# Performance work log

Measured on AMD Instinct MI355X. Metric: run time of the kernel, lower is better.

## Reference

```python
import jax, jax.numpy as jnp
import numpy as np

N_EMBD = 2048
N_HEAD = 16
N_KV_HEAD = 4
HD = N_EMBD // N_HEAD  # 128
B, T = 1, 4096
EPS = 1e-6


def apply_rope(x, cos, sin):
    # x: [B,T,H,hd]; cos/sin: [T,1,hd//2]
    hd = x.shape[-1] // 2
    x1, x2 = x[..., :hd], x[..., hd:]
    y1 = x1 * cos + x2 * sin
    y2 = x2 * cos - x1 * sin
    return jnp.concatenate((y1, y2), axis=-1).astype(x.dtype)


def rms_norm(x, eps=EPS):
    return x * jax.lax.rsqrt(jnp.mean(jnp.square(x), axis=-1, keepdims=True) + eps)


def setup_inputs() -> dict:
    key = jax.random.key(0)
    ks = jax.random.split(key, 7)
    s = 0.02
    return {
        "x": jax.random.normal(ks[0], (B, T, N_EMBD), dtype=jnp.float32),
        "cos": jax.random.normal(ks[1], (T, 1, HD // 2), dtype=jnp.float32),
        "sin": jax.random.normal(ks[2], (T, 1, HD // 2), dtype=jnp.float32),
        "wq": jax.random.normal(ks[3], (N_EMBD, N_HEAD * HD), dtype=jnp.float32) * s,
        "wk": jax.random.normal(ks[4], (N_EMBD, N_KV_HEAD * HD), dtype=jnp.float32) * s,
        "wv": jax.random.normal(ks[5], (N_EMBD, N_KV_HEAD * HD), dtype=jnp.float32) * s,
        "wo": jax.random.normal(ks[6], (N_EMBD, N_EMBD), dtype=jnp.float32) * s,
    }


def reference(x, cos, sin, wq, wk, wv, wo):
    Bb, Tt, C = x.shape
    q = (x @ wq).reshape(Bb, Tt, N_HEAD, HD)
    k = (x @ wk).reshape(Bb, Tt, N_KV_HEAD, HD)
    v = (x @ wv).reshape(Bb, Tt, N_KV_HEAD, HD)
    q = rms_norm(apply_rope(q, cos, sin))
    k = rms_norm(apply_rope(k, cos, sin))
    g = N_HEAD // N_KV_HEAD
    if g > 1:
        k = jnp.repeat(k, g, axis=2)  # [B,T,H,hd]
        v = jnp.repeat(v, g, axis=2)
    scale = 1.0 / jnp.sqrt(jnp.float32(HD))
    # scores: [B,H,T,S]
    scores = jnp.einsum("bthd,bshd->bhts", q, k) * scale
    causal = jnp.tril(jnp.ones((Tt, Tt), dtype=bool))
    scores = jnp.where(causal, scores, jnp.finfo(scores.dtype).min)
    attn = jax.nn.softmax(scores, axis=-1)
    y = jnp.einsum("bhts,bshd->bthd", attn, v).reshape(Bb, Tt, C)
    return y @ wo
```

## Files before the change

### kernel.cpp

```cpp
#include <hip/hip_runtime.h>

#define T_SEQ 4096
#define C_EMB 2048
#define NH 16
#define NKV 4
#define HD 128

typedef short bf16x8 __attribute__((ext_vector_type(8)));
typedef float f32x4 __attribute__((ext_vector_type(4)));
typedef unsigned short u16x4 __attribute__((ext_vector_type(4)));

__device__ inline unsigned short f2bf(float f) {
    unsigned int u = __float_as_uint(f);
    unsigned int r = (u + 0x7FFFu + ((u >> 16) & 1u)) >> 16;
    return (unsigned short)r;
}

__device__ __forceinline__ void async_cp16(const unsigned short* g, unsigned short* l) {
    __builtin_amdgcn_global_load_lds((const __attribute__((address_space(1))) unsigned int*)g,
                                     (__attribute__((address_space(3))) unsigned int*)l,
                                     16, 0, 0);
}

__global__ __launch_bounds__(256) void cvt_bf16(const float* __restrict__ in,
                                                unsigned short* __restrict__ out, int n) {
    int i = (blockIdx.x * 256 + threadIdx.x) * 4;
    if (i >= n) return;
    float4 f = *(const float4*)(&in[i]);
    u16x4 o;
    o.x = f2bf(f.x); o.y = f2bf(f.y); o.z = f2bf(f.z); o.w = f2bf(f.w);
    *(u16x4*)(&out[i]) = o;
}

__global__ __launch_bounds__(256) void transpose_all(const float* __restrict__ wq,
                                                     const float* __restrict__ wk,
                                                     const float* __restrict__ wv,
                                                     const float* __restrict__ wo,
                                                     unsigned short* __restrict__ wqkvT,
                                                     unsigned short* __restrict__ woT) {
    __shared__ float tile[32][33];
    int z = blockIdx.z;
    const float* in;
    unsigned short* out;
    int ld_in;
    if (z == 0)      { in = wq; out = wqkvT;                         ld_in = 2048; }
    else if (z == 1) { in = wk; out = wqkvT + (size_t)2048 * 2048;   ld_in = 512;  }
    else if (z == 2) { in = wv; out = wqkvT + (size_t)2560 * 2048;   ld_in = 512;  }
    else             { in = wo; out = woT;                           ld_in = 2048; }
    if ((z == 1 || z == 2) && blockIdx.x >= 16) return;

    int x = blockIdx.x * 32 + threadIdx.x;
    for (int i = threadIdx.y; i < 32; i += 8) {
        int y = blockIdx.y * 32 + i;
        tile[i][threadIdx.x] = in[(size_t)y * ld_in + x];
    }
    __syncthreads();
    int xo = blockIdx.y * 32 + threadIdx.x;
    for (int i = threadIdx.y; i < 32; i += 8) {
        int yo = blockIdx.x * 32 + i;
        out[(size_t)yo * 2048 + xo] = f2bf(tile[threadIdx.x][i]);
    }
}

__global__ __launch_bounds__(256, 4) void gemm_qkv(const unsigned short* __restrict__ A,
                                                   const unsigned short* __restrict__ Bt,
                                                   const float* __restrict__ cosb,
                                                   const float* __restrict__ sinb,
                                                   unsigned short* __restrict__ Qn,
                                                   unsigned short* __restrict__ Kn,
                                                   unsigned short* __restrict__ Vt) {
    __shared__ __align__(16) unsigned short As[2][128 * 32];
    __shared__ __align__(16) unsigned short Bs[2][128 * 32];
    const int K = 2048;
    int t = threadIdx.x;
    int w = t >> 6, lane = t & 63;
    int ln = lane & 15, q = lane >> 4;
    int wm = w * 32;
    int m0 = blockIdx.y * 128, n0 = blockIdx.x * 128;

    f32x4 acc[2][8] = {};

#pragma unroll
    for (int s = 0; s < 2; ++s) {
        int L = s * 256 + t;
        int r = L >> 2;
        int c = (L & 3) ^ ((L >> 4) & 3);
        async_cp16(&A[(size_t)(m0 + r) * K + c * 8], &As[0][s * 2048 + w * 512]);
        async_cp16(&Bt[(size_t)(n0 + r) * K + c * 8], &Bs[0][s * 2048 + w * 512]);
    }

    for (int it = 0; it < 64; ++it) {
        __syncthreads();
        if (it < 63) {
            int k0 = (it + 1) * 32;
            int p = (it + 1) & 1;
#pragma unroll
            for (int s = 0; s < 2; ++s) {
                int L = s * 256 + t;
                int r = L >> 2;
                int c = (L & 3) ^ ((L >> 4) & 3);
                async_cp16(&A[(size_t)(m0 + r) * K + k0 + c * 8], &As[p][s * 2048 + w * 512]);
                async_cp16(&Bt[(size_t)(n0 + r) * K + k0 + c * 8], &Bs[p][s * 2048 + w * 512]);
            }
        }
        int p = it & 1;
        int cs = (q ^ ((ln >> 2) & 3)) * 8;
        bf16x8 af[2], bfr[8];
#pragma unroll
        for (int i = 0; i < 2; ++i) af[i] = *(const bf16x8*)(&As[p][(wm + i * 16 + ln) * 32 + cs]);
#pragma unroll
        for (int j = 0; j < 8; ++j) bfr[j] = *(const bf16x8*)(&Bs[p][(j * 16 + ln) * 32 + cs]);
#pragma unroll
        for (int i = 0; i < 2; ++i)
#pragma unroll
            for (int j = 0; j < 8; ++j)
                acc[i][j] = __builtin_amdgcn_mfma_f32_16x16x32_bf16(af[i], bfr[j], acc[i][j], 0, 0, 0);
    }

    if (n0 < 2560) {
        bool isQ = (n0 < 2048);
        int h = isQ ? (n0 >> 7) : ((n0 - 2048) >> 7);
#pragma unroll
        for (int i = 0; i < 2; ++i)
#pragma unroll
            for (int r = 0; r < 4; ++r) {
                int row = m0 + wm + i * 16 + q * 4 + r;
                float y1[4], y2[4];
                float ss = 0.0f;
#pragma unroll
                for (int j = 0; j < 4; ++j) {
                    float a = acc[i][j][r];
                    float b = acc[i][j + 4][r];
                    float cc = cosb[row * 64 + j * 16 + ln];
                    float sv = sinb[row * 64 + j * 16 + ln];
                    y1[j] = a * cc + b * sv;
                    y2[j] = b * cc - a * sv;
                    ss += y1[j] * y1[j] + y2[j] * y2[j];
                }
                ss += __shfl_xor(ss, 1);
                ss += __shfl_xor(ss, 2);
                ss += __shfl_xor(ss, 4);
                ss += __shfl_xor(ss, 8);
                float rv = rsqrtf(ss * (1.0f / 128.0f) + 1e-6f);
                if (isQ) {
                    float s = rv * (0.08838834764831845f * 1.4426950408889634f);
                    unsigned short* ob = Qn + (size_t)row * 2048 + h * 128;
#pragma unroll
                    for (int j = 0; j < 4; ++j) {
                        ob[j * 16 + ln] = f2bf(y1[j] * s);
                        ob[64 + j * 16 + ln] = f2bf(y2[j] * s);
                    }
                } else {
                    unsigned short* ob = Kn + (size_t)row * 512 + h * 128;
#pragma unroll
                    for (int j = 0; j < 4; ++j) {
                        ob[j * 16 + ln] = f2bf(y1[j] * rv);
                        ob[64 + j * 16 + ln] = f2bf(y2[j] * rv);
                    }
                }
            }
    } else {
        int v0 = n0 - 2560;
        unsigned short* sm = &As[0][0];
#pragma unroll
        for (int half = 0; half < 2; ++half) {
            __syncthreads();
#pragma unroll
            for (int i = 0; i < 2; ++i)
#pragma unroll
                for (int jj = 0; jj < 4; ++jj) {
                    int j = half * 4 + jj;
                    int cc = jj * 16 + ln;
                    int rr = wm + i * 16 + q * 4;
                    u16x4 pk;
                    pk.x = f2bf(acc[i][j][0]); pk.y = f2bf(acc[i][j][1]);
                    pk.z = f2bf(acc[i][j][2]); pk.w = f2bf(acc[i][j][3]);
                    *(u16x4*)(&sm[cc * 136 + rr]) = pk;
                }
            __syncthreads();
            int vtr = t >> 2, mseg = (t & 3) * 32;
            unsigned short* dst = Vt + (size_t)(v0 + half * 64 + vtr) * 4096 + m0 + mseg;
            const unsigned short* src = &sm[vtr * 136 + mseg];
            *(int4*)(dst)      = *(const int4*)(src);
            *(int4*)(dst + 8)  = *(const int4*)(src + 8);
            *(int4*)(dst + 16) = *(const int4*)(src + 16);
            *(int4*)(dst + 24) = *(const int4*)(src + 24);
        }
    }
}

__global__ __launch_bounds__(256, 4) void gemm_bt_db(const unsigned short* __restrict__ A,
                                                     const unsigned short* __restrict__ Bt,
                                                     float* __restrict__ C, int M, int N, int K) {
    __shared__ __align__(16) unsigned short As[2][128 * 32];
    __shared__ __align__(16) unsigned short Bs[2][128 * 32];
    int t = threadIdx.x;
    int w = t >> 6, lane = t & 63;
    int ln = lane & 15, q = lane >> 4;
    int wm = (w >> 1) * 64, wn = (w & 1) * 64;
    int m0 = blockIdx.y * 128, n0 = blockIdx.x * 128;

    f32x4 acc[4][4] = {};

#pragma unroll
    for (int s = 0; s < 2; ++s) {
        int L = s * 256 + t;
        int r = L >> 2;
        int c = (L & 3) ^ ((L >> 4) & 3);
        async_cp16(&A[(size_t)(m0 + r) * K + c * 8], &As[0][s * 2048 + w * 512]);
        async_cp16(&Bt[(size_t)(n0 + r) * K + c * 8], &Bs[0][s * 2048 + w * 512]);
    }

    int niter = K >> 5;
    for (int it = 0; it < niter; ++it) {
        __syncthreads();
        if (it < niter - 1) {
            int k0 = (it + 1) * 32;
            int p = (it + 1) & 1;
#pragma unroll
            for (int s = 0; s < 2; ++s) {
                int L = s * 256 + t;
                int r = L >> 2;
                int c = (L & 3) ^ ((L >> 4) & 3);
                async_cp16(&A[(size_t)(m0 + r) * K + k0 + c * 8], &As[p][s * 2048 + w * 512]);
                async_cp16(&Bt[(size_t)(n0 + r) * K + k0 + c * 8], &Bs[p][s * 2048 + w * 512]);
            }
        }
        int p = it & 1;
        int cs = (q ^ ((ln >> 2) & 3)) * 8;
        bf16x8 af[4], bfr[4];
#pragma unroll
        for (int i = 0; i < 4; ++i) af[i] = *(const bf16x8*)(&As[p][(wm + i * 16 + ln) * 32 + cs]);
#pragma unroll
        for (int j = 0; j < 4; ++j) bfr[j] = *(const bf16x8*)(&Bs[p][(wn + j * 16 + ln) * 32 + cs]);
#pragma unroll
        for (int i = 0; i < 4; ++i)
#pragma unroll
            for (int j = 0; j < 4; ++j)
                acc[i][j] = __builtin_amdgcn_mfma_f32_16x16x32_bf16(af[i], bfr[j], acc[i][j], 0, 0, 0);
    }
#pragma unroll
    for (int i = 0; i < 4; ++i)
#pragma unroll
        for (int j = 0; j < 4; ++j)
#pragma unroll
            for (int r = 0; r < 4; ++r) {
                int row = m0 + wm + i * 16 + q * 4 + r;
                int col = n0 + wn + j * 16 + ln;
                C[(size_t)row * N + col] = acc[i][j][r];
            }
}

__global__ __launch_bounds__(256) void flash_attn(const unsigned short* __restrict__ Qn,
                                                  const unsigned short* __restrict__ Kn,
                                                  const unsigned short* __restrict__ Vt,
                                                  unsigned short* __restrict__ Ao) {
    __shared__ __align__(16) unsigned short Ks[2][64 * 128];
    __shared__ __align__(16) unsigned short Vs[2][128 * 64];
    __shared__ __align__(16) unsigned short Pl[4][16 * 72];

    int pairi = blockIdx.x;
    int h = blockIdx.y;
    int kvh = h >> 2;
    int t = threadIdx.x;
    int w = t >> 6, lane = t & 63;
    int ln = lane & 15, q = lane >> 4;

    int nA = 64 - pairi;
    int bq = 63 - pairi;
    int wq0 = bq * 64 + w * 16;

    bf16x8 qf[4];
    {
        const unsigned short* qb = Qn + (size_t)(wq0 + ln) * 2048 + h * 128;
#pragma unroll
        for (int kc = 0; kc < 4; ++kc) qf[kc] = *(const bf16x8*)(qb + kc * 32 + q * 8);
    }

    f32x4 o[8] = {};
    f32x4 l_p = {0.f, 0.f, 0.f, 0.f};

#pragma unroll
    for (int s = 0; s < 4; ++s) {
        int L = s * 256 + t;
        int key = L >> 4;
        int c = (L & 15) ^ (key & 15);
        async_cp16(Kn + (size_t)key * 512 + kvh * 128 + c * 8, &Ks[0][s * 2048 + w * 512]);
    }
#pragma unroll
    for (int s = 0; s < 4; ++s) {
        int L = s * 256 + t;
        int hd = L >> 3;
        int c = (L & 7) ^ (hd & 7);
        async_cp16(Vt + (size_t)(kvh * 128 + hd) * 4096 + c * 8, &Vs[0][s * 2048 + w * 512]);
    }

    for (int it = 0; it < 65; ++it) {
        __syncthreads();

        int nxt = it + 1;
        if (nxt < 65) {
            int nkt = (nxt < nA) ? nxt * 64 : (nxt - nA) * 64;
            unsigned short* kd = Ks[nxt & 1];
            unsigned short* vd = Vs[nxt & 1];
#pragma unroll
            for (int s = 0; s < 4; ++s) {
                int L = s * 256 + t;
                int key = L >> 4;
                int c = (L & 15) ^ (key & 15);
                async_cp16(Kn + (size_t)(nkt + key) * 512 + kvh * 128 + c * 8,
                           kd + s * 2048 + w * 512);
            }
#pragma unroll
            for (int s = 0; s < 4; ++s) {
                int L = s * 256 + t;
                int hd = L >> 3;
                int c = (L & 7) ^ (hd & 7);
                async_cp16(Vt + (size_t)(kvh * 128 + hd) * 4096 + nkt + c * 8,
                           vd + s * 2048 + w * 512);
            }
        }

        if (it == nA) {
#pragma unroll
            for (int r = 0; r < 4; ++r) {
                float lsum = l_p[r];
                lsum += __shfl_xor(lsum, 1);
                lsum += __shfl_xor(lsum, 2);
                lsum += __shfl_xor(lsum, 4);
                lsum += __shfl_xor(lsum, 8);
                float inv = 1.0f / lsum;
                int row = wq0 + q * 4 + r;
                unsigned short* ob = Ao + (size_t)row * 2048 + h * 128;
#pragma unroll
                for (int f = 0; f < 8; ++f) ob[f * 16 + ln] = f2bf(o[f][r] * inv);
            }
            bq = pairi;
            wq0 = bq * 64 + w * 16;
            const unsigned short* qb = Qn + (size_t)(wq0 + ln) * 2048 + h * 128;
#pragma unroll
            for (int kc = 0; kc < 4; ++kc) qf[kc] = *(const bf16x8*)(qb + kc * 32 + q * 8);
#pragma unroll
            for (int f = 0; f < 8; ++f) o[f] = (f32x4){0.f, 0.f, 0.f, 0.f};
            l_p = (f32x4){0.f, 0.f, 0.f, 0.f};
        }

        int kt0 = (it < nA) ? it * 64 : (it - nA) * 64;
        const unsigned short* kb = Ks[it & 1];
        const unsigned short* vb = Vs[it & 1];

        f32x4 sA[4] = {{-16.6f, -16.6f, -16.6f, -16.6f}, {-16.6f, -16.6f, -16.6f, -16.6f},
                       {-16.6f, -16.6f, -16.6f, -16.6f}, {-16.6f, -16.6f, -16.6f, -16.6f}};
#pragma unroll
        for (int jt = 0; jt < 4; ++jt) {
            int key = jt * 16 + ln;
#pragma unroll
            for (int kc = 0; kc < 4; ++kc) {
                int cs = ((kc * 4 + q) ^ ln) * 8;
                bf16x8 kf = *(const bf16x8*)(&kb[key * 128 + cs]);
                sA[jt] = __builtin_amdgcn_mfma_f32_16x16x32_bf16(qf[kc], kf, sA[jt], 0, 0, 0);
            }
        }
        if (kt0 + 63 > wq0) {
#pragma unroll
            for (int jt = 0; jt < 4; ++jt)
#pragma unroll
                for (int r = 0; r < 4; ++r) {
                    int key = kt0 + jt * 16 + ln;
                    int row = wq0 + q * 4 + r;
                    if (key > row) sA[jt][r] = -3e38f;
                }
        }
#pragma unroll
        for (int r = 0; r < 4; ++r) {
            int prow = (q * 4 + r) * 72;
#pragma unroll
            for (int jt = 0; jt < 4; ++jt) {
                float p = __builtin_amdgcn_exp2f(sA[jt][r]);
                Pl[w][prow + jt * 16 + ln] = (unsigned short)(__float_as_uint(p) >> 16);
                l_p[r] += p;
            }
        }

#pragma unroll
        for (int ks = 0; ks < 2; ++ks) {
            bf16x8 pa = *(const bf16x8*)(&Pl[w][ln * 72 + ks * 32 + q * 8]);
            int cs = ((ks * 4 + q) ^ (ln & 7)) * 8;
#pragma unroll
            for (int f = 0; f < 8; ++f) {
                bf16x8 vf = *(const bf16x8*)(&vb[(f * 16 + ln) * 64 + cs]);
                o[f] = __builtin_amdgcn_mfma_f32_16x16x32_bf16(pa, vf, o[f], 0, 0, 0);
            }
        }
    }
#pragma unroll
    for (int r = 0; r < 4; ++r) {
        float lsum = l_p[r];
        lsum += __shfl_xor(lsum, 1);
        lsum += __shfl_xor(lsum, 2);
        lsum += __shfl_xor(lsum, 4);
        lsum += __shfl_xor(lsum, 8);
        float inv = 1.0f / lsum;
        int row = wq0 + q * 4 + r;
        unsigned short* ob = Ao + (size_t)row * 2048 + h * 128;
#pragma unroll
        for (int f = 0; f < 8; ++f) ob[f * 16 + ln] = f2bf(o[f][r] * inv);
    }
}

extern "C" void kernel_launch(void* const* d_in, const int* in_sizes, int n_in,
                              void* d_out, int out_size, void* d_ws, size_t ws_size,
                              hipStream_t stream) {
    const float* x    = (const float*)d_in[0];
    const float* cosb = (const float*)d_in[1];
    const float* sinb = (const float*)d_in[2];
    const float* wq   = (const float*)d_in[3];
    const float* wk   = (const float*)d_in[4];
    const float* wv   = (const float*)d_in[5];
    const float* wo   = (const float*)d_in[6];
    float* out = (float*)d_out;

    char* ws = (char*)d_ws;
    unsigned short* xb    = (unsigned short*)ws;
    unsigned short* wqkvT = xb    + (size_t)4096 * 2048;
    unsigned short* woT   = wqkvT + (size_t)3072 * 2048;
    unsigned short* Qn    = woT   + (size_t)2048 * 2048;
    unsigned short* Kn    = Qn    + (size_t)4096 * 2048;
    unsigned short* Vt    = Kn    + (size_t)4096 * 512;
    unsigned short* Ao    = Vt    + (size_t)512 * 4096;

    cvt_bf16<<<(4096 * 2048 / 4 + 255) / 256, 256, 0, stream>>>(x, xb, 4096 * 2048);
    transpose_all<<<dim3(64, 64, 4), dim3(32, 8), 0, stream>>>(wq, wk, wv, wo, wqkvT, woT);
    gemm_qkv<<<dim3(24, 32), 256, 0, stream>>>(xb, wqkvT, cosb, sinb, Qn, Kn, Vt);
    flash_attn<<<dim3(32, 16), 256, 0, stream>>>(Qn, Kn, Vt, Ao);
    gemm_bt_db<<<dim3(16, 32), 256, 0, stream>>>(Ao, woT, out, 4096, 2048, 2048);
}
```

Before: 357.5 us.

## Make each attention wave own 32 query rows with 2 waves per block

The flash attention kernel now runs 128 threads (2 waves) per block, and each wave handles 32 query rows as two 16-row sub-tiles instead of one. Every K and V fragment read from LDS is reused across two MFMAs, which halves LDS read traffic per unit of compute. The cost is twice the accumulator and Q registers per wave, only two waves per block to hide latency, and each thread issuing twice as many async copies. The grid is unchanged at 512 blocks, so each CU has fewer waves resident.

```diff
diff --git a/kernel.cpp b/kernel.cpp
--- a/kernel.cpp
+++ b/kernel.cpp
@@ -251,13 +251,13 @@
             }
 }
 
-__global__ __launch_bounds__(256) void flash_attn(const unsigned short* __restrict__ Qn,
+__global__ __launch_bounds__(128) void flash_attn(const unsigned short* __restrict__ Qn,
                                                   const unsigned short* __restrict__ Kn,
                                                   const unsigned short* __restrict__ Vt,
                                                   unsigned short* __restrict__ Ao) {
     __shared__ __align__(16) unsigned short Ks[2][64 * 128];
     __shared__ __align__(16) unsigned short Vs[2][128 * 64];
-    __shared__ __align__(16) unsigned short Pl[4][16 * 72];
+    __shared__ __align__(16) unsigned short Pl[2][32 * 72];
 
     int pairi = blockIdx.x;
     int h = blockIdx.y;
@@ -268,31 +268,32 @@
 
     int nA = 64 - pairi;
     int bq = 63 - pairi;
-    int wq0 = bq * 64 + w * 16;
-
-    bf16x8 qf[4];
-    {
-        const unsigned short* qb = Qn + (size_t)(wq0 + ln) * 2048 + h * 128;
-#pragma unroll
-        for (int kc = 0; kc < 4; ++kc) qf[kc] = *(const bf16x8*)(qb + kc * 32 + q * 8);
-    }
-
-    f32x4 o[8] = {};
-    f32x4 l_p = {0.f, 0.f, 0.f, 0.f};
-
-#pragma unroll
-    for (int s = 0; s < 4; ++s) {
-        int L = s * 256 + t;
+    int wq0 = bq * 64 + w * 32;
+
+    bf16x8 qf[2][4];
+#pragma unroll
+    for (int i = 0; i < 2; ++i) {
+        const unsigned short* qb = Qn + (size_t)(wq0 + i * 16 + ln) * 2048 + h * 128;
+#pragma unroll
+        for (int kc = 0; kc < 4; ++kc) qf[i][kc] = *(const bf16x8*)(qb + kc * 32 + q * 8);
+    }
+
+    f32x4 o[2][8] = {};
+    f32x4 l_p[2] = {};
+
+#pragma unroll
+    for (int s = 0; s < 8; ++s) {
+        int L = s * 128 + t;
         int key = L >> 4;
         int c = (L & 15) ^ (key & 15);
-        async_cp16(Kn + (size_t)key * 512 + kvh * 128 + c * 8, &Ks[0][s * 2048 + w * 512]);
-    }
-#pragma unroll
-    for (int s = 0; s < 4; ++s) {
-        int L = s * 256 + t;
+        async_cp16(Kn + (size_t)key * 512 + kvh * 128 + c * 8, &Ks[0][s * 1024 + w * 512]);
+    }
+#pragma unroll
+    for (int s = 0; s < 8; ++s) {
+        int L = s * 128 + t;
         int hd = L >> 3;
         int c = (L & 7) ^ (hd & 7);
-        async_cp16(Vt + (size_t)(kvh * 128 + hd) * 4096 + c * 8, &Vs[0][s * 2048 + w * 512]);
+        async_cp16(Vt + (size_t)(kvh * 128 + hd) * 4096 + c * 8, &Vs[0][s * 1024 + w * 512]);
     }
 
     for (int it = 0; it < 65; ++it) {
@@ -304,53 +305,66 @@
             unsigned short* kd = Ks[nxt & 1];
             unsigned short* vd = Vs[nxt & 1];
 #pragma unroll
-            for (int s = 0; s < 4; ++s) {
-                int L = s * 256 + t;
+            for (int s = 0; s < 8; ++s) {
+                int L = s * 128 + t;
                 int key = L >> 4;
                 int c = (L & 15) ^ (key & 15);
                 async_cp16(Kn + (size_t)(nkt + key) * 512 + kvh * 128 + c * 8,
-                           kd + s * 2048 + w * 512);
-            }
-#pragma unroll
-            for (int s = 0; s < 4; ++s) {
-                int L = s * 256 + t;
+                           kd + s * 1024 + w * 512);
+            }
+#pragma unroll
+            for (int s = 0; s < 8; ++s) {
+                int L = s * 128 + t;
                 int hd = L >> 3;
                 int c = (L & 7) ^ (hd & 7);
                 async_cp16(Vt + (size_t)(kvh * 128 + hd) * 4096 + nkt + c * 8,
-                           vd + s * 2048 + w * 512);
+                           vd + s * 1024 + w * 512);
             }
         }
 
         if (it == nA) {
 #pragma unroll
-            for (int r = 0; r < 4; ++r) {
-                float lsum = l_p[r];
-                lsum += __shfl_xor(lsum, 1);
-                lsum += __shfl_xor(lsum, 2);
-                lsum += __shfl_xor(lsum, 4);
-                lsum += __shfl_xor(lsum, 8);
-                float inv = 1.0f / lsum;
-                int row = wq0 + q * 4 + r;
-                unsigned short* ob = Ao + (size_t)row * 2048 + h * 128;
-#pragma unroll
-                for (int f = 0; f < 8; ++f) ob[f * 16 + ln] = f2bf(o[f][r] * inv);
-            }
+            for (int i = 0; i < 2; ++i)
+#pragma unroll
+                for (int r = 0; r < 4; ++r) {
+                    float lsum = l_p[i][r];
+                    lsum += __shfl_xor(lsum, 1);
+                    lsum += __shfl_xor(lsum, 2);
+                    lsum += __shfl_xor(lsum, 4);
+                    lsum += __shfl_xor(lsum, 8);
+                    float inv = 1.0f / lsum;
+                    int row = wq0 + i * 16 + q * 4 + r;
+                    unsigned short* ob = Ao + (size_t)row * 2048 + h * 128;
+#pragma unroll
+                    for (int f = 0; f < 8; ++f) ob[f * 16 + ln] = f2bf(o[i][f][r] * inv);
+                }
             bq = pairi;
-            wq0 = bq * 64 + w * 16;
-            const unsigned short* qb = Qn + (size_t)(wq0 + ln) * 2048 + h * 128;
-#pragma unroll
-            for (int kc = 0; kc < 4; ++kc) qf[kc] = *(const bf16x8*)(qb + kc * 32 + q * 8);
-#pragma unroll
-            for (int f = 0; f < 8; ++f) o[f] = (f32x4){0.f, 0.f, 0.f, 0.f};
-            l_p = (f32x4){0.f, 0.f, 0.f, 0.f};
+            wq0 = bq * 64 + w * 32;
+#pragma unroll
+            for (int i = 0; i < 2; ++i) {
+                const unsigned short* qb = Qn + (size_t)(wq0 + i * 16 + ln) * 2048 + h * 128;
+#pragma unroll
+                for (int kc = 0; kc < 4; ++kc) qf[i][kc] = *(const bf16x8*)(qb + kc * 32 + q * 8);
+            }
+#pragma unroll
+            for (int i = 0; i < 2; ++i) {
+#pragma unroll
+                for (int f = 0; f < 8; ++f) o[i][f] = (f32x4){0.f, 0.f, 0.f, 0.f};
+                l_p[i] = (f32x4){0.f, 0.f, 0.f, 0.f};
+            }
         }
 
         int kt0 = (it < nA) ? it * 64 : (it - nA) * 64;
         const unsigned short* kb = Ks[it & 1];
         const unsigned short* vb = Vs[it & 1];
 
-        f32x4 sA[4] = {{-16.6f, -16.6f, -16.6f, -16.6f}, {-16.6f, -16.6f, -16.6f, -16.6f},
-                       {-16.6f, -16.6f, -16.6f, -16.6f}, {-16.6f, -16.6f, -16.6f, -16.6f}};
+        f32x4 sA[2][4];
+#pragma unroll
+        for (int i = 0; i < 2; ++i)
+#pragma unroll
+            for (int jt = 0; jt < 4; ++jt)
+                sA[i][jt] = (f32x4){-16.6f, -16.6f, -16.6f, -16.6f};
+
 #pragma unroll
         for (int jt = 0; jt < 4; ++jt) {
             int key = jt * 16 + ln;
@@ -358,54 +372,63 @@
             for (int kc = 0; kc < 4; ++kc) {
                 int cs = ((kc * 4 + q) ^ ln) * 8;
                 bf16x8 kf = *(const bf16x8*)(&kb[key * 128 + cs]);
-                sA[jt] = __builtin_amdgcn_mfma_f32_16x16x32_bf16(qf[kc], kf, sA[jt], 0, 0, 0);
+                sA[0][jt] = __builtin_amdgcn_mfma_f32_16x16x32_bf16(qf[0][kc], kf, sA[0][jt], 0, 0, 0);
+                sA[1][jt] = __builtin_amdgcn_mfma_f32_16x16x32_bf16(qf[1][kc], kf, sA[1][jt], 0, 0, 0);
             }
         }
         if (kt0 + 63 > wq0) {
 #pragma unroll
-            for (int jt = 0; jt < 4; ++jt)
-#pragma unroll
-                for (int r = 0; r < 4; ++r) {
-                    int key = kt0 + jt * 16 + ln;
-                    int row = wq0 + q * 4 + r;
-                    if (key > row) sA[jt][r] = -3e38f;
+            for (int i = 0; i < 2; ++i)
+#pragma unroll
+                for (int jt = 0; jt < 4; ++jt)
+#pragma unroll
+                    for (int r = 0; r < 4; ++r) {
+                        int key = kt0 + jt * 16 + ln;
+                        int row = wq0 + i * 16 + q * 4 + r;
+                        if (key > row) sA[i][jt][r] = -3e38f;
+                    }
+        }
+#pragma unroll
+        for (int i = 0; i < 2; ++i)
+#pragma unroll
+            for (int r = 0; r < 4; ++r) {
+                int prow = (i * 16 + q * 4 + r) * 72;
+#pragma unroll
+                for (int jt = 0; jt < 4; ++jt) {
+                    float p = __builtin_amdgcn_exp2f(sA[i][jt][r]);
+                    Pl[w][prow + jt * 16 + ln] = (unsigned short)(__float_as_uint(p) >> 16);
+                    l_p[i][r] += p;
                 }
-        }
-#pragma unroll
-        for (int r = 0; r < 4; ++r) {
-            int prow = (q * 4 + r) * 72;
-#pragma unroll
-            for (int jt = 0; jt < 4; ++jt) {
-                float p = __builtin_amdgcn_exp2f(sA[jt][r]);
-                Pl[w][prow + jt * 16 + ln] = (unsigned short)(__float_as_uint(p) >> 16);
-                l_p[r] += p;
-            }
-        }
+            }
 
 #pragma unroll
         for (int ks = 0; ks < 2; ++ks) {
-            bf16x8 pa = *(const bf16x8*)(&Pl[w][ln * 72 + ks * 32 + q * 8]);
+            bf16x8 pa0 = *(const bf16x8*)(&Pl[w][ln * 72 + ks * 32 + q * 8]);
+            bf16x8 pa1 = *(const bf16x8*)(&Pl[w][(16 + ln) * 72 + ks * 32 + q * 8]);
             int cs = ((ks * 4 + q) ^ (ln & 7)) * 8;
 #pragma unroll
             for (int f = 0; f < 8; ++f) {
                 bf16x8 vf = *(const bf16x8*)(&vb[(f * 16 + ln) * 64 + cs]);
-                o[f] = __builtin_amdgcn_mfma_f32_16x16x32_bf16(pa, vf, o[f], 0, 0, 0);
-            }
-        }
-    }
-#pragma unroll
-    for (int r = 0; r < 4; ++r) {
-        float lsum = l_p[r];
-        lsum += __shfl_xor(lsum, 1);
-        lsum += __shfl_xor(lsum, 2);
-        lsum += __shfl_xor(lsum, 4);
-        lsum += __shfl_xor(lsum, 8);
-        float inv = 1.0f / lsum;
-        int row = wq0 + q * 4 + r;
-        unsigned short* ob = Ao + (size_t)row * 2048 + h * 128;
-#pragma unroll
-        for (int f = 0; f < 8; ++f) ob[f * 16 + ln] = f2bf(o[f][r] * inv);
-    }
+                o[0][f] = __builtin_amdgcn_mfma_f32_16x16x32_bf16(pa0, vf, o[0][f], 0, 0, 0);
+                o[1][f] = __builtin_amdgcn_mfma_f32_16x16x32_bf16(pa1, vf, o[1][f], 0, 0, 0);
+            }
+        }
+    }
+#pragma unroll
+    for (int i = 0; i < 2; ++i)
+#pragma unroll
+        for (int r = 0; r < 4; ++r) {
+            float lsum = l_p[i][r];
+            lsum += __shfl_xor(lsum, 1);
+            lsum += __shfl_xor(lsum, 2);
+            lsum += __shfl_xor(lsum, 4);
+            lsum += __shfl_xor(lsum, 8);
+            float inv = 1.0f / lsum;
+            int row = wq0 + i * 16 + q * 4 + r;
+            unsigned short* ob = Ao + (size_t)row * 2048 + h * 128;
+#pragma unroll
+            for (int f = 0; f < 8; ++f) ob[f * 16 + ln] = f2bf(o[i][f][r] * inv);
+        }
 }
 
 extern "C" void kernel_launch(void* const* d_in, const int* in_sizes, int n_in,
@@ -432,6 +455,6 @@
     cvt_bf16<<<(4096 * 2048 / 4 + 255) / 256, 256, 0, stream>>>(x, xb, 4096 * 2048);
     transpose_all<<<dim3(64, 64, 4), dim3(32, 8), 0, stream>>>(wq, wk, wv, wo, wqkvT, woT);
     gemm_qkv<<<dim3(24, 32), 256, 0, stream>>>(xb, wqkvT, cosb, sinb, Qn, Kn, Vt);
-    flash_attn<<<dim3(32, 16), 256, 0, stream>>>(Qn, Kn, Vt, Ao);
+    flash_attn<<<dim3(32, 16), 128, 0, stream>>>(Qn, Kn, Vt, Ao);
     gemm_bt_db<<<dim3(16, 32), 256, 0, stream>>>(Ao, woT, out, 4096, 2048, 2048);
 }
```

New measurement: 399.0 us. +11.6%, slower.
